# Kernel optimization log

Measured on AMD Instinct MI355X. Metric: run time of the kernel, lower is better.

Reference implementation:

```python
import jax, jax.numpy as jnp
import numpy as np
from jax import lax

T = 4096  # time length; conv widths 4094->1023->255->84 (even) so view(-1,30) works

def relu6(v):
    return jnp.clip(v, 0.0, 6.0)

def setup_inputs() -> dict:
    key = jax.random.key(0)
    ks = jax.random.split(key, 20)
    s = 0.25  # ~ torch default init scale for fan_in 16
    x = jax.random.normal(ks[0], (1, 1, 18, T), dtype=jnp.float32)
    # 4 stacked Linear(16,16) per cross-modal block: [Q, Kin, Vin, QKVout]
    cm1_W = jax.random.normal(ks[1], (4, 16, 16), dtype=jnp.float32) * s
    cm1_b = jax.random.normal(ks[2], (4, 16), dtype=jnp.float32) * s
    cm2_W = jax.random.normal(ks[3], (4, 16, 16), dtype=jnp.float32) * s
    cm2_b = jax.random.normal(ks[4], (4, 16), dtype=jnp.float32) * s
    cw0 = jax.random.normal(ks[5], (5, 1, 2, 3), dtype=jnp.float32) * 0.3
    cw1 = jax.random.normal(ks[6], (5, 5, 2, 4), dtype=jnp.float32) * 0.15
    cw2 = jax.random.normal(ks[7], (5, 5, 2, 4), dtype=jnp.float32) * 0.15
    cw3 = jax.random.normal(ks[8], (5, 5, 2, 4), dtype=jnp.float32) * 0.15
    cb = jax.random.normal(ks[9], (4, 5), dtype=jnp.float32) * 0.1
    fc1_W = jax.random.normal(ks[10], (15, 30), dtype=jnp.float32) * 0.18
    fc1_b = jax.random.normal(ks[11], (15,), dtype=jnp.float32) * 0.18
    fc2_W = jax.random.normal(ks[12], (2, 15), dtype=jnp.float32) * 0.25
    fc2_b = jax.random.normal(ks[13], (2,), dtype=jnp.float32) * 0.25
    return dict(x=x, cm1_W=cm1_W, cm1_b=cm1_b, cm2_W=cm2_W, cm2_b=cm2_b,
                cw0=cw0, cw1=cw1, cw2=cw2, cw3=cw3, cb=cb,
                fc1_W=fc1_W, fc1_b=fc1_b, fc2_W=fc2_W, fc2_b=fc2_b)

def _cm(wav_row, eeg2, W, b):
    # wav_row: [T], eeg2: [16, T]; W: [4,16,16], b: [4,16]
    wavP = wav_row[None, :] * eeg2          # [16, T]   (wav * eeg broadcast)
    mat = eeg2.T @ wavP                     # [T, T]
    wavP = wavP @ mat                       # [16, T]
    w = wavP.T                              # [T, 16]
    e = eeg2.T                              # [T, 16]
    Q = relu6(e @ W[0].T + b[0])            # [T, 16]
    K = relu6(w @ W[1].T + b[1])
    V = relu6(w @ W[2].T + b[2])
    # Softmax2d on [T,T,1,1] == softmax over axis 1 (per-row over keys)
    A = jax.nn.softmax(Q @ K.T, axis=1)     # [T, T]
    # Softmax2d on [T,16,1,1] == softmax over the 16 features per row
    S = jax.nn.softmax(A @ V, axis=1)       # [T, 16]
    out = relu6(S @ W[3].T + b[3])          # [T, 16]
    return out.T                            # [16, T]

def reference(x, cm1_W, cm1_b, cm2_W, cm2_b, cw0, cw1, cw2, cw3, cb,
              fc1_W, fc1_b, fc2_W, fc2_b):
    eeg2 = x[0, 0, 1:-1, :]                 # [16, T]
    wavA = _cm(x[0, 0, 0, :], eeg2, cm1_W, cm1_b)   # [16, T]
    wavB = _cm(x[0, 0, -1, :], eeg2, cm2_W, cm2_b)  # [16, T]
    y = jnp.concatenate([wavA, eeg2, wavB], axis=0)[None, None]  # [1,1,48,T]
    dn = ('NCHW', 'OIHW', 'NCHW')
    y = relu6(lax.conv_general_dilated(y, cw0, (2, 1), 'VALID', dimension_numbers=dn) + cb[0][None, :, None, None])
    y = relu6(lax.conv_general_dilated(y, cw1, (2, 4), 'VALID', dimension_numbers=dn) + cb[1][None, :, None, None])
    y = relu6(lax.conv_general_dilated(y, cw2, (2, 4), 'VALID', dimension_numbers=dn) + cb[2][None, :, None, None])
    y = relu6(lax.conv_general_dilated(y, cw3, (2, 3), 'VALID', dimension_numbers=dn) + cb[3][None, :, None, None])
    y = y.reshape(-1, 30)                   # [42, 30]
    h = jax.nn.sigmoid(y @ fc1_W.T + fc1_b) # [42, 15]
    out = jax.nn.softmax(h @ fc2_W.T + fc2_b, axis=1)  # [42, 2]
    return out
```

## Files before the change

### kernel.cpp

```cpp
#include <hip/hip_runtime.h>

#define TT 4096
#define KS 8

#define OFF_GPART 0
#define OFF_QH    32768
#define OFF_QL    98304
#define OFF_KH    163840
#define OFF_KL    229376
#define OFF_VT    294912
#define OFF_Y     360448
#define OFF_P     557056
#define OFF_C1    557056
#define OFF_C2    618496

typedef __attribute__((ext_vector_type(8))) short short8;
typedef __attribute__((ext_vector_type(4))) float f32x4;

__device__ __forceinline__ float relu6f(float v){ return fminf(fmaxf(v, 0.f), 6.f); }
__device__ __forceinline__ unsigned short f2bf(float f){
  unsigned int u = __float_as_uint(f);
  return (unsigned short)((u + 0x7FFFu + ((u>>16)&1u)) >> 16);
}
__device__ __forceinline__ float bf2f(unsigned short s){
  return __uint_as_float(((unsigned int)s)<<16);
}

__global__ __launch_bounds__(256) void k_gpart(const float* __restrict__ x, float* __restrict__ ws){
  const int b = blockIdx.x, tid = threadIdx.x;
  const int i = tid >> 4, j = tid & 15;
  const int t0 = b*64;
  const float4* ei4 = reinterpret_cast<const float4*>(x + (size_t)(1+i)*TT + t0);
  const float4* ej4 = reinterpret_cast<const float4*>(x + (size_t)(1+j)*TT + t0);
  const float4* wA4 = reinterpret_cast<const float4*>(x + t0);
  const float4* wB4 = reinterpret_cast<const float4*>(x + (size_t)17*TT + t0);
  float gA = 0.f, gB = 0.f;
  #pragma unroll 4
  for (int u = 0; u < 16; ++u){
    float4 a = ei4[u], c = ej4[u], wa = wA4[u], wb = wB4[u];
    float p0 = a.x*c.x, p1 = a.y*c.y, p2 = a.z*c.z, p3 = a.w*c.w;
    gA = fmaf(wa.x, p0, gA); gA = fmaf(wa.y, p1, gA); gA = fmaf(wa.z, p2, gA); gA = fmaf(wa.w, p3, gA);
    gB = fmaf(wb.x, p0, gB); gB = fmaf(wb.y, p1, gB); gB = fmaf(wb.z, p2, gB); gB = fmaf(wb.w, p3, gB);
  }
  ws[OFF_GPART + (size_t)tid*64 + b]         = gA;
  ws[OFF_GPART + (size_t)(256+tid)*64 + b]   = gB;
}

__global__ __launch_bounds__(128) void k_qkv(const float* __restrict__ x,
    const float* __restrict__ cm1W, const float* __restrict__ cm1b,
    const float* __restrict__ cm2W, const float* __restrict__ cm2b,
    float* __restrict__ ws){
  __shared__ float4 sG4[64];
  __shared__ float4 sW0[64], sW1[64], sW2[64];
  __shared__ float sB[48];
  const int b = blockIdx.x;
  const int cm = b >> 5;
  const int tid = threadIdx.x;
  {
    const float4* g4a = reinterpret_cast<const float4*>(ws + OFF_GPART + (size_t)(cm*256 + tid)*64);
    const float4* g4b = reinterpret_cast<const float4*>(ws + OFF_GPART + (size_t)(cm*256 + 128 + tid)*64);
    float g0 = 0.f, g1 = 0.f;
    #pragma unroll
    for (int u = 0; u < 16; ++u){
      float4 a = g4a[u], c = g4b[u];
      g0 += (a.x + a.y) + (a.z + a.w);
      g1 += (c.x + c.y) + (c.z + c.w);
    }
    ((float*)sG4)[tid]       = g0;
    ((float*)sG4)[tid + 128] = g1;
  }
  const float* W  = cm ? cm2W : cm1W;
  const float* Bb = cm ? cm2b : cm1b;
  ((float*)sW0)[tid]       = W[tid];
  ((float*)sW0)[tid + 128] = W[tid + 128];
  ((float*)sW1)[tid]       = W[256 + tid];
  ((float*)sW1)[tid + 128] = W[384 + tid];
  ((float*)sW2)[tid]       = W[512 + tid];
  ((float*)sW2)[tid + 128] = W[640 + tid];
  if (tid < 48) sB[tid] = Bb[tid];
  __syncthreads();

  const int t = (b & 31)*128 + tid;
  float e[16], p[16], w2[16];
  const float wav = x[(size_t)(cm ? 17 : 0)*TT + t];
  #pragma unroll
  for (int d = 0; d < 16; ++d){ e[d] = x[(size_t)(1+d)*TT + t]; p[d] = wav * e[d]; }

  #pragma unroll
  for (int c = 0; c < 16; ++c){
    float a = 0.f;
    #pragma unroll
    for (int dv = 0; dv < 4; ++dv){
      float4 gv = sG4[c*4+dv];
      a = fmaf(gv.x, p[4*dv+0], a); a = fmaf(gv.y, p[4*dv+1], a);
      a = fmaf(gv.z, p[4*dv+2], a); a = fmaf(gv.w, p[4*dv+3], a);
    }
    w2[c] = a;
  }
  float q[16], kk[16], vv[16];
  #pragma unroll
  for (int c = 0; c < 16; ++c){
    float aq = sB[c], ak = sB[16+c], av = sB[32+c];
    #pragma unroll
    for (int dv = 0; dv < 4; ++dv){
      float4 w0 = sW0[c*4+dv], w1 = sW1[c*4+dv], w3 = sW2[c*4+dv];
      aq = fmaf(w0.x, e[4*dv+0], aq);  aq = fmaf(w0.y, e[4*dv+1], aq);
      aq = fmaf(w0.z, e[4*dv+2], aq);  aq = fmaf(w0.w, e[4*dv+3], aq);
      ak = fmaf(w1.x, w2[4*dv+0], ak); ak = fmaf(w1.y, w2[4*dv+1], ak);
      ak = fmaf(w1.z, w2[4*dv+2], ak); ak = fmaf(w1.w, w2[4*dv+3], ak);
      av = fmaf(w3.x, w2[4*dv+0], av); av = fmaf(w3.y, w2[4*dv+1], av);
      av = fmaf(w3.z, w2[4*dv+2], av); av = fmaf(w3.w, w2[4*dv+3], av);
    }
    q[c] = relu6f(aq); kk[c] = relu6f(ak); vv[c] = relu6f(av);
  }
  unsigned short qhv[16], qlv[16], khv[16], klv[16];
  #pragma unroll
  for (int d = 0; d < 16; ++d){
    qhv[d] = f2bf(q[d]);  qlv[d] = f2bf(q[d]  - bf2f(qhv[d]));
    khv[d] = f2bf(kk[d]); klv[d] = f2bf(kk[d] - bf2f(khv[d]));
  }
  const size_t rowus = ((size_t)cm*TT + t)*16;
  unsigned int wq[8];
  #pragma unroll
  for (int xx = 0; xx < 8; ++xx) wq[xx] = (unsigned int)qhv[2*xx] | ((unsigned int)qhv[2*xx+1]<<16);
  ((uint4*)((unsigned short*)(ws+OFF_QH)+rowus))[0] = make_uint4(wq[0],wq[1],wq[2],wq[3]);
  ((uint4*)((unsigned short*)(ws+OFF_QH)+rowus))[1] = make_uint4(wq[4],wq[5],wq[6],wq[7]);
  #pragma unroll
  for (int xx = 0; xx < 8; ++xx) wq[xx] = (unsigned int)qlv[2*xx] | ((unsigned int)qlv[2*xx+1]<<16);
  ((uint4*)((unsigned short*)(ws+OFF_QL)+rowus))[0] = make_uint4(wq[0],wq[1],wq[2],wq[3]);
  ((uint4*)((unsigned short*)(ws+OFF_QL)+rowus))[1] = make_uint4(wq[4],wq[5],wq[6],wq[7]);
  #pragma unroll
  for (int xx = 0; xx < 8; ++xx) wq[xx] = (unsigned int)khv[2*xx] | ((unsigned int)khv[2*xx+1]<<16);
  ((uint4*)((unsigned short*)(ws+OFF_KH)+rowus))[0] = make_uint4(wq[0],wq[1],wq[2],wq[3]);
  ((uint4*)((unsigned short*)(ws+OFF_KH)+rowus))[1] = make_uint4(wq[4],wq[5],wq[6],wq[7]);
  #pragma unroll
  for (int xx = 0; xx < 8; ++xx) wq[xx] = (unsigned int)klv[2*xx] | ((unsigned int)klv[2*xx+1]<<16);
  ((uint4*)((unsigned short*)(ws+OFF_KL)+rowus))[0] = make_uint4(wq[0],wq[1],wq[2],wq[3]);
  ((uint4*)((unsigned short*)(ws+OFF_KL)+rowus))[1] = make_uint4(wq[4],wq[5],wq[6],wq[7]);
  unsigned short* vtp = (unsigned short*)(ws+OFF_VT) + (size_t)cm*16*TT;
  #pragma unroll
  for (int d = 0; d < 16; ++d) vtp[(size_t)d*TT + t] = f2bf(vv[d]);

  if (cm == 0){
    #pragma unroll
    for (int d = 0; d < 16; ++d) ws[OFF_Y + (size_t)(16+d)*TT + t] = e[d];
  }
}

__global__ __launch_bounds__(256) void k_attn_main(float* __restrict__ ws){
  const int unit = blockIdx.x*4 + (threadIdx.x >> 6);
  const int lane = threadIdx.x & 63;
  const int cm = unit >> 11;
  const int rem = unit & 2047;
  const int qt = rem >> 3;
  const int ks = rem & 7;
  const int i = lane & 15, g = lane >> 4;

  const unsigned short* qh = (const unsigned short*)(ws + OFF_QH) + (size_t)cm*TT*16;
  const unsigned short* ql = (const unsigned short*)(ws + OFF_QL) + (size_t)cm*TT*16;
  const unsigned short* kh = (const unsigned short*)(ws + OFF_KH) + (size_t)cm*TT*16;
  const unsigned short* kl = (const unsigned short*)(ws + OFF_KL) + (size_t)cm*TT*16;
  const unsigned short* vt = (const unsigned short*)(ws + OFF_VT) + (size_t)cm*16*TT;

  const short8 zero8 = {0,0,0,0,0,0,0,0};
  short8 bqh = zero8, bql = zero8;
  if (g < 2){
    bqh = *(const short8*)(qh + ((size_t)(qt*16 + i))*16 + g*8);
    bql = *(const short8*)(ql + ((size_t)(qt*16 + i))*16 + g*8);
  }
  const int key0 = ks*512;
  const int keyA = ((i>>2)<<3) + (i&3);
  f32x4 acc = {0.f,0.f,0.f,0.f};
  float lsum = 0.f;

  for (int t = 0; t < 16; ++t){
    const int k0 = key0 + t*32;
    short8 a0h = zero8, a0l = zero8, a1h = zero8, a1l = zero8;
    if (g < 2){
      a0h = *(const short8*)(kh + ((size_t)(k0 + keyA))*16 + g*8);
      a0l = *(const short8*)(kl + ((size_t)(k0 + keyA))*16 + g*8);
      a1h = *(const short8*)(kh + ((size_t)(k0 + keyA + 4))*16 + g*8);
      a1l = *(const short8*)(kl + ((size_t)(k0 + keyA + 4))*16 + g*8);
    }
    f32x4 d0 = {0.f,0.f,0.f,0.f}, d1 = {0.f,0.f,0.f,0.f};
    d0 = __builtin_amdgcn_mfma_f32_16x16x32_bf16(a0h, bqh, d0, 0,0,0);
    d0 = __builtin_amdgcn_mfma_f32_16x16x32_bf16(a0h, bql, d0, 0,0,0);
    d0 = __builtin_amdgcn_mfma_f32_16x16x32_bf16(a0l, bqh, d0, 0,0,0);
    d1 = __builtin_amdgcn_mfma_f32_16x16x32_bf16(a1h, bqh, d1, 0,0,0);
    d1 = __builtin_amdgcn_mfma_f32_16x16x32_bf16(a1h, bql, d1, 0,0,0);
    d1 = __builtin_amdgcn_mfma_f32_16x16x32_bf16(a1l, bqh, d1, 0,0,0);
    float p0[4], p1[4];
    #pragma unroll
    for (int r = 0; r < 4; ++r){ p0[r] = __expf(fminf(d0[r],100.f) - 32.f); lsum += p0[r]; }
    #pragma unroll
    for (int r = 0; r < 4; ++r){ p1[r] = __expf(fminf(d1[r],100.f) - 32.f); lsum += p1[r]; }
    short8 pa;
    pa[0]=(short)f2bf(p0[0]); pa[1]=(short)f2bf(p0[1]); pa[2]=(short)f2bf(p0[2]); pa[3]=(short)f2bf(p0[3]);
    pa[4]=(short)f2bf(p1[0]); pa[5]=(short)f2bf(p1[1]); pa[6]=(short)f2bf(p1[2]); pa[7]=(short)f2bf(p1[3]);
    short8 bv = *(const short8*)(vt + (size_t)i*TT + k0 + g*8);
    acc = __builtin_amdgcn_mfma_f32_16x16x32_bf16(pa, bv, acc, 0,0,0);
  }
  lsum += __shfl_xor(lsum, 16);
  lsum += __shfl_xor(lsum, 32);
  float* Pb = ws + OFF_P + (size_t)((cm*KS + ks)*17)*TT;
  if (lane < 16) Pb[qt*16 + lane] = lsum;
  #pragma unroll
  for (int r = 0; r < 4; ++r)
    Pb[(size_t)(1 + i)*TT + qt*16 + g*4 + r] = acc[r];
}

__global__ __launch_bounds__(256) void k_attn_sum(float* __restrict__ ws){
  const int idx = blockIdx.x*256 + threadIdx.x;
  if (idx >= 2*17*TT) return;
  const int cm = idx / (17*TT);
  const int r  = idx - cm*17*TT;
  const float* Pb = ws + OFF_P + (size_t)cm*KS*17*TT + r;
  float s = 0.f;
  #pragma unroll
  for (int k = 0; k < KS; ++k) s += Pb[(size_t)k*17*TT];
  ws[OFF_P + (size_t)cm*KS*17*TT + r] = s;
}

__global__ __launch_bounds__(128) void k_attn_epi(
    const float* __restrict__ cm1W, const float* __restrict__ cm1b,
    const float* __restrict__ cm2W, const float* __restrict__ cm2b,
    float* __restrict__ ws){
  const int gid = blockIdx.x*128 + threadIdx.x;
  const int cm = gid >> 12;
  const int q = gid & 4095;
  const float* Mb = ws + OFF_P + (size_t)cm*KS*17*TT + q;
  const float lt = Mb[0];
  float a[16];
  #pragma unroll
  for (int d = 0; d < 16; ++d) a[d] = Mb[(size_t)(1+d)*TT];
  const float invl = 1.f/lt;
  float mx = -1e30f;
  #pragma unroll
  for (int d = 0; d < 16; ++d){ a[d] *= invl; mx = fmaxf(mx, a[d]); }
  float es = 0.f;
  #pragma unroll
  for (int d = 0; d < 16; ++d){ a[d] = __expf(a[d]-mx); es += a[d]; }
  const float invs = 1.f/es;
  const float* W  = cm ? cm2W : cm1W;
  const float* Bb = cm ? cm2b : cm1b;
  #pragma unroll
  for (int c = 0; c < 16; ++c){
    float o = 0.f;
    #pragma unroll
    for (int d = 0; d < 16; ++d) o = fmaf(W[768 + c*16 + d], a[d], o);
    o = relu6f(fmaf(o, invs, Bb[48 + c]));
    ws[OFF_Y + (size_t)((cm ? 32 : 0) + c)*TT + q] = o;
  }
}

__global__ __launch_bounds__(256) void k_conv01(const float* __restrict__ cw0,
    const float* __restrict__ cw1, const float* __restrict__ cb, float* __restrict__ ws){
  const int idx = blockIdx.x*256 + threadIdx.x;
  const int WO = 1023, HO = 12;
  if (idx >= 5*HO*WO) return;
  const int ow = idx % WO; int tmp = idx / WO;
  const int oh = tmp % HO; const int oc = tmp / HO;
  const float* y = ws + OFF_Y;
  float yp[4][7];
  #pragma unroll
  for (int r = 0; r < 4; ++r){
    const float* yr = y + (size_t)(4*oh + r)*TT + 4*ow;
    #pragma unroll
    for (int cx = 0; cx < 7; ++cx) yp[r][cx] = yr[cx];
  }
  float a = cb[5 + oc];
  #pragma unroll
  for (int ic = 0; ic < 5; ++ic){
    const float* w0 = cw0 + ic*6;
    const float* w1 = cw1 + ((oc*5+ic)*2)*4;
    #pragma unroll
    for (int kh = 0; kh < 2; ++kh){
      #pragma unroll
      for (int kw = 0; kw < 4; ++kw){
        float c0 = cb[ic];
        c0 = fmaf(w0[0], yp[2*kh][kw],   c0);
        c0 = fmaf(w0[1], yp[2*kh][kw+1], c0);
        c0 = fmaf(w0[2], yp[2*kh][kw+2], c0);
        c0 = fmaf(w0[3], yp[2*kh+1][kw],   c0);
        c0 = fmaf(w0[4], yp[2*kh+1][kw+1], c0);
        c0 = fmaf(w0[5], yp[2*kh+1][kw+2], c0);
        c0 = relu6f(c0);
        a = fmaf(w1[kh*4+kw], c0, a);
      }
    }
  }
  ws[OFF_C1 + idx] = relu6f(a);
}

__global__ __launch_bounds__(256) void k_conv2(const float* __restrict__ cw2,
    const float* __restrict__ cb, float* __restrict__ ws){
  const int idx = blockIdx.x*256 + threadIdx.x;
  if (idx >= 5*6*255) return;
  const int ow = idx % 255; int tmp = idx/255;
  const int oh = tmp % 6; const int oc = tmp/6;
  const float* c1 = ws + OFF_C1;
  float a = cb[10 + oc];
  #pragma unroll
  for (int ic = 0; ic < 5; ++ic)
    #pragma unroll
    for (int kh = 0; kh < 2; ++kh)
      #pragma unroll
      for (int kw = 0; kw < 4; ++kw)
        a = fmaf(cw2[((oc*5+ic)*2+kh)*4+kw], c1[(size_t)(ic*12 + 2*oh+kh)*1023 + 4*ow+kw], a);
  ws[OFF_C2 + idx] = relu6f(a);
}

__global__ __launch_bounds__(256) void k_tail(
    const float* __restrict__ cw3, const float* __restrict__ cb,
    const float* __restrict__ fc1W, const float* __restrict__ fc1b,
    const float* __restrict__ fc2W, const float* __restrict__ fc2b,
    const float* __restrict__ ws, float* __restrict__ out){
  __shared__ float c2[5*6*255];
  __shared__ float c3[5*3*84];
  __shared__ float hsm[42*15];
  const int tid = threadIdx.x;
  for (int i = tid; i < 5*6*255; i += 256) c2[i] = ws[OFF_C2 + i];
  __syncthreads();
  for (int idx = tid; idx < 5*3*84; idx += 256){
    const int ow = idx % 84; int tmp = idx/84;
    const int oh = tmp % 3; const int oc = tmp/3;
    float a = cb[15 + oc];
    #pragma unroll
    for (int ic = 0; ic < 5; ++ic)
      #pragma unroll
      for (int kh = 0; kh < 2; ++kh)
        #pragma unroll
        for (int kw = 0; kw < 4; ++kw)
          a = fmaf(cw3[((oc*5+ic)*2+kh)*4+kw], c2[(ic*6 + 2*oh+kh)*255 + 3*ow+kw], a);
    c3[idx] = relu6f(a);
  }
  __syncthreads();
  for (int i = tid; i < 630; i += 256){
    const int s = i / 15, kx = i % 15;
    const float* row = c3 + s*30;
    float a = fc1b[kx];
    #pragma unroll
    for (int n = 0; n < 30; ++n) a = fmaf(fc1W[kx*30+n], row[n], a);
    hsm[i] = 1.f/(1.f + __expf(-a));
  }
  __syncthreads();
  if (tid < 42){
    const float* h = hsm + tid*15;
    float l0 = fc2b[0], l1 = fc2b[1];
    #pragma unroll
    for (int kx = 0; kx < 15; ++kx){
      l0 = fmaf(fc2W[kx],    h[kx], l0);
      l1 = fmaf(fc2W[15+kx], h[kx], l1);
    }
    float mx = fmaxf(l0, l1);
    float e0 = __expf(l0-mx), e1 = __expf(l1-mx);
    float s = e0 + e1;
    out[tid*2]   = e0/s;
    out[tid*2+1] = e1/s;
  }
}

extern "C" void kernel_launch(void* const* d_in, const int* in_sizes, int n_in,
                              void* d_out, int out_size, void* d_ws, size_t ws_size,
                              hipStream_t stream){
  const float* x    = (const float*)d_in[0];
  const float* cm1W = (const float*)d_in[1];
  const float* cm1b = (const float*)d_in[2];
  const float* cm2W = (const float*)d_in[3];
  const float* cm2b = (const float*)d_in[4];
  const float* cw0  = (const float*)d_in[5];
  const float* cw1  = (const float*)d_in[6];
  const float* cw2  = (const float*)d_in[7];
  const float* cw3  = (const float*)d_in[8];
  const float* cb   = (const float*)d_in[9];
  const float* fc1W = (const float*)d_in[10];
  const float* fc1b = (const float*)d_in[11];
  const float* fc2W = (const float*)d_in[12];
  const float* fc2b = (const float*)d_in[13];
  float* ws  = (float*)d_ws;
  float* out = (float*)d_out;

  k_gpart    <<<dim3(64),   dim3(256), 0, stream>>>(x, ws);
  k_qkv      <<<dim3(64),   dim3(128), 0, stream>>>(x, cm1W, cm1b, cm2W, cm2b, ws);
  k_attn_main<<<dim3(1024), dim3(256), 0, stream>>>(ws);
  k_attn_sum <<<dim3(544),  dim3(256), 0, stream>>>(ws);
  k_attn_epi <<<dim3(64),   dim3(128), 0, stream>>>(cm1W, cm1b, cm2W, cm2b, ws);
  k_conv01   <<<dim3(240),  dim3(256), 0, stream>>>(cw0, cw1, cb, ws);
  k_conv2    <<<dim3(30),   dim3(256), 0, stream>>>(cw2, cb, ws);
  k_tail     <<<dim3(1),    dim3(256), 0, stream>>>(cw3, cb, fc1W, fc1b, fc2W, fc2b, ws, out);
}
```

Before: 58.64 us.

## Process two query tiles per wave and pack hi/lo K splits into one MFMA

Each wave now handles 32 queries (two 16-query tiles) instead of 16, so every K and V fragment load is reused across both tiles, and the launch grid is halved. The split-bf16 QK product is restructured so lanes g<2 carry K-high and lanes g>=2 carry K-low, with Q hi/lo in the matching halves. That folds the three MFMAs per block into two per tile and removes the zero padding that left half of each K=32 MFMA empty. Register pressure rises and the grid has fewer waves, which may reduce latency hiding.

```diff
diff --git a/kernel.cpp b/kernel.cpp
--- a/kernel.cpp
+++ b/kernel.cpp
@@ -150,63 +150,77 @@
 __global__ __launch_bounds__(256) void k_attn_main(float* __restrict__ ws){
   const int unit = blockIdx.x*4 + (threadIdx.x >> 6);
   const int lane = threadIdx.x & 63;
-  const int cm = unit >> 11;
-  const int rem = unit & 2047;
-  const int qt = rem >> 3;
+  const int cm = unit >> 10;
+  const int rem = unit & 1023;
+  const int qt2 = rem >> 3;
   const int ks = rem & 7;
   const int i = lane & 15, g = lane >> 4;
+  const int gb = (g & 1) * 8;
 
   const unsigned short* qh = (const unsigned short*)(ws + OFF_QH) + (size_t)cm*TT*16;
   const unsigned short* ql = (const unsigned short*)(ws + OFF_QL) + (size_t)cm*TT*16;
   const unsigned short* kh = (const unsigned short*)(ws + OFF_KH) + (size_t)cm*TT*16;
   const unsigned short* kl = (const unsigned short*)(ws + OFF_KL) + (size_t)cm*TT*16;
   const unsigned short* vt = (const unsigned short*)(ws + OFF_VT) + (size_t)cm*16*TT;
-
-  const short8 zero8 = {0,0,0,0,0,0,0,0};
-  short8 bqh = zero8, bql = zero8;
-  if (g < 2){
-    bqh = *(const short8*)(qh + ((size_t)(qt*16 + i))*16 + g*8);
-    bql = *(const short8*)(ql + ((size_t)(qt*16 + i))*16 + g*8);
-  }
+  const unsigned short* kbase = (g < 2) ? kh : kl;
+
+  const int qA = qt2*32 + i, qB = qA + 16;
+  const short8 b1A = *(const short8*)(qh + (size_t)qA*16 + gb);
+  const short8 b2A = *(const short8*)(ql + (size_t)qA*16 + gb);
+  const short8 b1B = *(const short8*)(qh + (size_t)qB*16 + gb);
+  const short8 b2B = *(const short8*)(ql + (size_t)qB*16 + gb);
+
   const int key0 = ks*512;
   const int keyA = ((i>>2)<<3) + (i&3);
-  f32x4 acc = {0.f,0.f,0.f,0.f};
-  float lsum = 0.f;
+  f32x4 accA = {0.f,0.f,0.f,0.f}, accB = {0.f,0.f,0.f,0.f};
+  float lsumA = 0.f, lsumB = 0.f;
 
   for (int t = 0; t < 16; ++t){
     const int k0 = key0 + t*32;
-    short8 a0h = zero8, a0l = zero8, a1h = zero8, a1l = zero8;
-    if (g < 2){
-      a0h = *(const short8*)(kh + ((size_t)(k0 + keyA))*16 + g*8);
-      a0l = *(const short8*)(kl + ((size_t)(k0 + keyA))*16 + g*8);
-      a1h = *(const short8*)(kh + ((size_t)(k0 + keyA + 4))*16 + g*8);
-      a1l = *(const short8*)(kl + ((size_t)(k0 + keyA + 4))*16 + g*8);
-    }
-    f32x4 d0 = {0.f,0.f,0.f,0.f}, d1 = {0.f,0.f,0.f,0.f};
-    d0 = __builtin_amdgcn_mfma_f32_16x16x32_bf16(a0h, bqh, d0, 0,0,0);
-    d0 = __builtin_amdgcn_mfma_f32_16x16x32_bf16(a0h, bql, d0, 0,0,0);
-    d0 = __builtin_amdgcn_mfma_f32_16x16x32_bf16(a0l, bqh, d0, 0,0,0);
-    d1 = __builtin_amdgcn_mfma_f32_16x16x32_bf16(a1h, bqh, d1, 0,0,0);
-    d1 = __builtin_amdgcn_mfma_f32_16x16x32_bf16(a1h, bql, d1, 0,0,0);
-    d1 = __builtin_amdgcn_mfma_f32_16x16x32_bf16(a1l, bqh, d1, 0,0,0);
-    float p0[4], p1[4];
-    #pragma unroll
-    for (int r = 0; r < 4; ++r){ p0[r] = __expf(fminf(d0[r],100.f) - 32.f); lsum += p0[r]; }
-    #pragma unroll
-    for (int r = 0; r < 4; ++r){ p1[r] = __expf(fminf(d1[r],100.f) - 32.f); lsum += p1[r]; }
-    short8 pa;
-    pa[0]=(short)f2bf(p0[0]); pa[1]=(short)f2bf(p0[1]); pa[2]=(short)f2bf(p0[2]); pa[3]=(short)f2bf(p0[3]);
-    pa[4]=(short)f2bf(p1[0]); pa[5]=(short)f2bf(p1[1]); pa[6]=(short)f2bf(p1[2]); pa[7]=(short)f2bf(p1[3]);
-    short8 bv = *(const short8*)(vt + (size_t)i*TT + k0 + g*8);
-    acc = __builtin_amdgcn_mfma_f32_16x16x32_bf16(pa, bv, acc, 0,0,0);
-  }
-  lsum += __shfl_xor(lsum, 16);
-  lsum += __shfl_xor(lsum, 32);
+    const short8 a0 = *(const short8*)(kbase + ((size_t)(k0 + keyA))*16 + gb);
+    const short8 a1 = *(const short8*)(kbase + ((size_t)(k0 + keyA + 4))*16 + gb);
+    f32x4 d0A = {0.f,0.f,0.f,0.f}, d1A = {0.f,0.f,0.f,0.f};
+    f32x4 d0B = {0.f,0.f,0.f,0.f}, d1B = {0.f,0.f,0.f,0.f};
+    d0A = __builtin_amdgcn_mfma_f32_16x16x32_bf16(a0, b1A, d0A, 0,0,0);
+    d0A = __builtin_amdgcn_mfma_f32_16x16x32_bf16(a0, b2A, d0A, 0,0,0);
+    d1A = __builtin_amdgcn_mfma_f32_16x16x32_bf16(a1, b1A, d1A, 0,0,0);
+    d1A = __builtin_amdgcn_mfma_f32_16x16x32_bf16(a1, b2A, d1A, 0,0,0);
+    d0B = __builtin_amdgcn_mfma_f32_16x16x32_bf16(a0, b1B, d0B, 0,0,0);
+    d0B = __builtin_amdgcn_mfma_f32_16x16x32_bf16(a0, b2B, d0B, 0,0,0);
+    d1B = __builtin_amdgcn_mfma_f32_16x16x32_bf16(a1, b1B, d1B, 0,0,0);
+    d1B = __builtin_amdgcn_mfma_f32_16x16x32_bf16(a1, b2B, d1B, 0,0,0);
+    float p0A[4], p1A[4], p0B[4], p1B[4];
+    #pragma unroll
+    for (int r = 0; r < 4; ++r){
+      p0A[r] = __expf(fminf(d0A[r],100.f) - 32.f); lsumA += p0A[r];
+      p1A[r] = __expf(fminf(d1A[r],100.f) - 32.f); lsumA += p1A[r];
+      p0B[r] = __expf(fminf(d0B[r],100.f) - 32.f); lsumB += p0B[r];
+      p1B[r] = __expf(fminf(d1B[r],100.f) - 32.f); lsumB += p1B[r];
+    }
+    short8 paA, paB;
+    #pragma unroll
+    for (int r = 0; r < 4; ++r){
+      paA[r]   = (short)f2bf(p0A[r]);
+      paA[r+4] = (short)f2bf(p1A[r]);
+      paB[r]   = (short)f2bf(p0B[r]);
+      paB[r+4] = (short)f2bf(p1B[r]);
+    }
+    const short8 bv = *(const short8*)(vt + (size_t)i*TT + k0 + g*8);
+    accA = __builtin_amdgcn_mfma_f32_16x16x32_bf16(paA, bv, accA, 0,0,0);
+    accB = __builtin_amdgcn_mfma_f32_16x16x32_bf16(paB, bv, accB, 0,0,0);
+  }
+  lsumA += __shfl_xor(lsumA, 16);  lsumA += __shfl_xor(lsumA, 32);
+  lsumB += __shfl_xor(lsumB, 16);  lsumB += __shfl_xor(lsumB, 32);
   float* Pb = ws + OFF_P + (size_t)((cm*KS + ks)*17)*TT;
-  if (lane < 16) Pb[qt*16 + lane] = lsum;
-  #pragma unroll
-  for (int r = 0; r < 4; ++r)
-    Pb[(size_t)(1 + i)*TT + qt*16 + g*4 + r] = acc[r];
+  if (lane < 16){
+    Pb[qt2*32 + lane]      = lsumA;
+    Pb[qt2*32 + 16 + lane] = lsumB;
+  }
+  #pragma unroll
+  for (int r = 0; r < 4; ++r){
+    Pb[(size_t)(1 + i)*TT + qt2*32 + g*4 + r]      = accA[r];
+    Pb[(size_t)(1 + i)*TT + qt2*32 + 16 + g*4 + r] = accB[r];
+  }
 }
 
 __global__ __launch_bounds__(256) void k_attn_sum(float* __restrict__ ws){
@@ -380,12 +394,12 @@
   float* ws  = (float*)d_ws;
   float* out = (float*)d_out;
 
-  k_gpart    <<<dim3(64),   dim3(256), 0, stream>>>(x, ws);
-  k_qkv      <<<dim3(64),   dim3(128), 0, stream>>>(x, cm1W, cm1b, cm2W, cm2b, ws);
-  k_attn_main<<<dim3(1024), dim3(256), 0, stream>>>(ws);
-  k_attn_sum <<<dim3(544),  dim3(256), 0, stream>>>(ws);
-  k_attn_epi <<<dim3(64),   dim3(128), 0, stream>>>(cm1W, cm1b, cm2W, cm2b, ws);
-  k_conv01   <<<dim3(240),  dim3(256), 0, stream>>>(cw0, cw1, cb, ws);
-  k_conv2    <<<dim3(30),   dim3(256), 0, stream>>>(cw2, cb, ws);
-  k_tail     <<<dim3(1),    dim3(256), 0, stream>>>(cw3, cb, fc1W, fc1b, fc2W, fc2b, ws, out);
-}
+  k_gpart    <<<dim3(64),  dim3(256), 0, stream>>>(x, ws);
+  k_qkv      <<<dim3(64),  dim3(128), 0, stream>>>(x, cm1W, cm1b, cm2W, cm2b, ws);
+  k_attn_main<<<dim3(512), dim3(256), 0, stream>>>(ws);
+  k_attn_sum <<<dim3(544), dim3(256), 0, stream>>>(ws);
+  k_attn_epi <<<dim3(64),  dim3(128), 0, stream>>>(cm1W, cm1b, cm2W, cm2b, ws);
+  k_conv01   <<<dim3(240), dim3(256), 0, stream>>>(cw0, cw1, cb, ws);
+  k_conv2    <<<dim3(30),  dim3(256), 0, stream>>>(cw2, cb, ws);
+  k_tail     <<<dim3(1),   dim3(256), 0, stream>>>(cw3, cb, fc1W, fc1b, fc2W, fc2b, ws, out);
+}
```

After: 56.89 us. 1.03x faster.
